# Kernel tuning notes

Hardware: AMD Instinct MI355X
Metric: run time of the kernel (lower is better)

Reference implementation:

```python
import jax, jax.numpy as jnp
import numpy as np

GAMMA = 0.01  # matches init_kwargs gamma
BIG = 1e10    # matches tf.fill(..., 10000000000.0)


def _softmin(vals, gamma):
    # soft-min with softmin weights (my_min in the original): stable log-sum-exp
    z = -vals / gamma
    lse = jax.nn.logsumexp(z)
    return -gamma * lse, jnp.exp(z - lse)


def dtw_grad(theta, gamma):
    """Soft-DTW forward DP + backward E-recursion for one cost matrix theta [m, n].
    Returns E[1:m+1, 1:n+1] (the soft alignment / gradient matrix), shape [m, n]."""
    m, n = theta.shape

    # ---- forward DP: V[i, j] = theta[i-1, j-1] + softmin(V[i,j-1], V[i-1,j-1], V[i-1,j])
    def row_step(prev_row, theta_row):
        # prev_row = V[i-1, 0:n+1]
        def col_step(v_left, inp):
            th, v_diag, v_up = inp
            min_val, w = _softmin(jnp.stack([v_left, v_diag, v_up]), gamma)
            v = th + min_val
            return v, (v, w)
        _, (v_row, q_row) = jax.lax.scan(
            col_step, jnp.float32(BIG), (theta_row, prev_row[:-1], prev_row[1:]))
        new_row = jnp.concatenate([jnp.full((1,), BIG, theta.dtype), v_row])
        return new_row, q_row

    init_row = jnp.full((n + 1,), BIG, theta.dtype).at[0].set(0.0)  # V[0,0]=0
    _, Q_rows = jax.lax.scan(row_step, init_row, theta)  # Q_rows: (m, n, 3)

    # pad Q to (m+2, n+2, 3), Q[m+1, n+1] = [1,1,1]
    Q = (jnp.zeros((m + 2, n + 2, 3), theta.dtype)
         .at[1:m + 1, 1:n + 1].set(Q_rows)
         .at[m + 1, n + 1].set(1.0))

    # ---- backward: E[i,j] = Q[i,j+1,0]E[i,j+1] + Q[i+1,j+1,1]E[i+1,j+1] + Q[i+1,j,2]E[i+1,j]
    def brow_step(e_next, rows):
        # e_next = E[i+1, 0:n+2]; rows = (Q[i], Q[i+1]) each (n+2, 3)
        q_i, q_ip1 = rows
        # j runs n..1 (reverse order along columns)
        xs = (q_i[2:, 0][::-1],        # Q[i, j+1, 0]
              q_ip1[2:, 1][::-1],      # Q[i+1, j+1, 1]
              q_ip1[1:n + 1, 2][::-1], # Q[i+1, j, 2]
              e_next[2:][::-1],        # E[i+1, j+1]
              e_next[1:n + 1][::-1])   # E[i+1, j]

        def bcol_step(e_right, x):
            a, b, c, e1, e2 = x
            e = a * e_right + b * e1 + c * e2
            return e, e

        _, e_rev = jax.lax.scan(bcol_step, jnp.float32(0.0), xs)
        e_inner = e_rev[::-1]  # E[i, 1:n+1]
        e_row = jnp.zeros((n + 2,), theta.dtype).at[1:n + 1].set(e_inner)
        return e_row, e_inner

    e_init = jnp.zeros((n + 2,), theta.dtype).at[n + 1].set(1.0)  # E[m+1, n+1] = 1
    _, E_rev = jax.lax.scan(brow_step, e_init, (Q[m:0:-1], Q[m + 1:1:-1]))
    return E_rev[::-1]  # (m, n)


def setup_inputs() -> dict:
    key = jax.random.key(0)
    # D: batch of pairwise cost matrices, non-negative
    D = jax.random.uniform(key, (64, 256, 256), dtype=jnp.float32)
    return {"D": D}


def reference(D):
    E = jax.vmap(lambda t: dtw_grad(t, GAMMA))(D)  # (B, N, N)
    return jnp.mean(E, axis=0)
```

## Files before the change

kernel.cpp:

```cpp
#include <hip/hip_runtime.h>


#define MM 256
#define NN 256
#define R 2
#define NB 64
#define NBLK 128
#define NVL 128
#define SBIG 1.0e12f
#define K2   144.269504089f

__device__ __forceinline__ float f4get(const float4& v, int k) {
    switch (k) { case 0: return v.x; case 1: return v.y; case 2: return v.z; default: return v.w; }
}
__device__ __forceinline__ int iclamp(int x, int lo, int hi) {
    return x < lo ? lo : (x > hi ? hi : x);
}
__device__ __forceinline__ void lds_barrier() {
    asm volatile("s_waitcnt lgkmcnt(0)\n\ts_barrier" ::: "memory");
}

template<bool REV>
__device__ __forceinline__ void run_dp(const float* __restrict__ th,
                                       float* __restrict__ Vp,
                                       float4 (*xb)[NVL + 1])
{
    const int L = threadIdx.x;

    float vprev[R];
    #pragma unroll
    for (int r = 0; r < R; ++r) vprev[r] = SBIG;
    float4 rec = make_float4(SBIG, SBIG, SBIG, SBIG);
    float prevW = SBIG;
    float4 botV4 = make_float4(SBIG, SBIG, SBIG, SBIG);
    float4 thB[3][R];
    #pragma unroll
    for (int p = 0; p < 3; ++p)
        #pragma unroll
        for (int r = 0; r < R; ++r) thB[p][r] = make_float4(0.f, 0.f, 0.f, 0.f);

    if (threadIdx.x == 0) {
        xb[0][0] = make_float4(SBIG, SBIG, SBIG, SBIG);
        xb[1][0] = make_float4(SBIG, SBIG, SBIG, SBIG);
    }
    __syncthreads();

    auto body = [&](const int LD, const int CU, const int m) {
        const int g = m - L;
        const int gl = iclamp(g + 2, 0, 63);
        #pragma unroll
        for (int r = 0; r < R; ++r) {
            const int vr = 2 * L + r;
            if (REV) {
                const float4 t = *(const float4*)(th + (255 - vr) * NN + (252 - 4 * gl));
                thB[LD][r] = make_float4(t.w, t.z, t.y, t.x);
            } else {
                thB[LD][r] = *(const float4*)(th + vr * NN + 4 * gl);
            }
        }
        if (g >= 0 && g <= 63) {
            const float4 topV = rec;
            const float vd0 = (g == 0) ? ((L == 0) ? 0.0f : SBIG) : prevW;
            float vbuf[R][4];
            #pragma unroll
            for (int cc = 0; cc < 4; ++cc) {
                float vu = f4get(topV, cc);
                float vd = (cc == 0) ? vd0 : f4get(topV, cc - 1);
                #pragma unroll
                for (int r = 0; r < R; ++r) {
                    const float vl = vprev[r];
                    const float mn = fminf(vl, fminf(vd, vu));
                    const float el = exp2f(mn - vl);
                    const float ed = exp2f(mn - vd);
                    const float eu = exp2f(mn - vu);
                    const float ss = el + ed + eu;
                    const float a  = mn - log2f(ss);
                    const float v  = fmaf(f4get(thB[CU][r], cc), K2, a);
                    vbuf[r][cc] = v;
                    vd = vl;
                    vu = v;
                    vprev[r] = v;
                }
            }
            botV4 = make_float4(vbuf[R - 1][0], vbuf[R - 1][1], vbuf[R - 1][2], vbuf[R - 1][3]);
            #pragma unroll
            for (int r = 0; r < R; ++r) {
                const int vr = 2 * L + r;
                if (REV)
                    *(float4*)(Vp + (255 - vr) * NN + (252 - 4 * g)) =
                        make_float4(vbuf[r][3], vbuf[r][2], vbuf[r][1], vbuf[r][0]);
                else
                    *(float4*)(Vp + vr * NN + 4 * g) =
                        make_float4(vbuf[r][0], vbuf[r][1], vbuf[r][2], vbuf[r][3]);
            }
        }
        xb[m & 1][L + 1] = botV4;
        lds_barrier();
        prevW = rec.w;
        rec = xb[m & 1][L];
    };
    for (int k = 0; k < 195; k += 3) {
        body(0, 1, k - 2);
        body(1, 2, k - 1);
        body(2, 0, k);
    }
}

__global__ __launch_bounds__(128) void dtw_fb(
    const float* __restrict__ D,
    float* __restrict__ out,
    float* __restrict__ ws)
{
    __shared__ float4 xb[2][NVL + 1];

    const int blk = blockIdx.x;
    const bool rev = blk >= NB;
    const int b = rev ? blk - NB : blk;
    const float* __restrict__ th = D + (size_t)b * (MM * NN);
    float* __restrict__ Fp = ws + (size_t)b * (MM * NN);
    float* __restrict__ Bp = ws + (size_t)(NB + b) * (MM * NN);
    unsigned* ctr = (unsigned*)(ws + (size_t)2 * NB * (MM * NN));

    if (rev) run_dp<true >(th, Bp, xb);
    else     run_dp<false>(th, Fp, xb);

    __syncthreads();
    __threadfence();
    __syncthreads();
    if (threadIdx.x == 0)
        __hip_atomic_fetch_add(ctr, 1u, __ATOMIC_ACQ_REL, __HIP_MEMORY_SCOPE_AGENT);
    unsigned cnt;
    do {
        cnt = __hip_atomic_load(ctr, __ATOMIC_ACQUIRE, __HIP_MEMORY_SCOPE_AGENT);
        if (cnt < NBLK) __builtin_amdgcn_s_sleep(2);
    } while (cnt < NBLK);
    __builtin_amdgcn_fence(__ATOMIC_ACQUIRE, "agent");

    {
        const int row = 2 * blk + (threadIdx.x >> 6);
        const int col = 4 * (threadIdx.x & 63);
        const size_t off = (size_t)row * NN + col;
        float4 acc = make_float4(0.f, 0.f, 0.f, 0.f);
        for (int p = 0; p < NB; ++p) {
            const float* __restrict__ thp = D + (size_t)p * (MM * NN);
            const float* __restrict__ fp  = ws + (size_t)p * (MM * NN);
            const float* __restrict__ bp  = ws + (size_t)(NB + p) * (MM * NN);
            const float Ft = fp[MM * NN - 1];
            const float4 t4 = *(const float4*)(thp + off);
            const float4 f4 = *(const float4*)(fp + off);
            const float4 b4 = *(const float4*)(bp + off);
            acc.x += exp2f(fmaf(t4.x, K2, (Ft - f4.x) - b4.x));
            acc.y += exp2f(fmaf(t4.y, K2, (Ft - f4.y) - b4.y));
            acc.z += exp2f(fmaf(t4.z, K2, (Ft - f4.z) - b4.z));
            acc.w += exp2f(fmaf(t4.w, K2, (Ft - f4.w) - b4.w));
        }
        const float inv = 1.0f / (float)NB;
        *(float4*)(out + off) =
            make_float4(acc.x * inv, acc.y * inv, acc.z * inv, acc.w * inv);
    }
}

extern "C" void kernel_launch(void* const* d_in, const int* in_sizes, int n_in,
                              void* d_out, int out_size, void* d_ws, size_t ws_size,
                              hipStream_t stream) {
    const float* D = (const float*)d_in[0];
    float* out = (float*)d_out;
    float* ws = (float*)d_ws;

    hipMemsetAsync(ws + (size_t)2 * NB * (MM * NN), 0, sizeof(unsigned), stream);
    dtw_fb<<<dim3(NBLK), dim3(128), 0, stream>>>(D, out, ws);
}
```

Before: 235.9 us.

## Shrink DP to one wavefront with four rows per lane and shuffle handoff

The wavefront DP now runs in a single 64-lane wavefront per block, with each lane owning four rows instead of two. Rows pass between neighbouring lanes through __shfl_up instead of an LDS buffer and block-wide barriers. This cuts the pipeline length from 195 to 129 steps and removes barrier cost on the serial critical path, but each lane now does twice the sequential work per step. The final reduction is reorganised so each thread handles two float4 column chunks to match the smaller block.

```diff
diff --git a/kernel.cpp b/kernel.cpp
--- a/kernel.cpp
+++ b/kernel.cpp
@@ -3,10 +3,9 @@
 
 #define MM 256
 #define NN 256
-#define R 2
+#define R 4
 #define NB 64
 #define NBLK 128
-#define NVL 128
 #define SBIG 1.0e12f
 #define K2   144.269504089f
 
@@ -16,14 +15,10 @@
 __device__ __forceinline__ int iclamp(int x, int lo, int hi) {
     return x < lo ? lo : (x > hi ? hi : x);
 }
-__device__ __forceinline__ void lds_barrier() {
-    asm volatile("s_waitcnt lgkmcnt(0)\n\ts_barrier" ::: "memory");
-}
 
 template<bool REV>
 __device__ __forceinline__ void run_dp(const float* __restrict__ th,
-                                       float* __restrict__ Vp,
-                                       float4 (*xb)[NVL + 1])
+                                       float* __restrict__ Vp)
 {
     const int L = threadIdx.x;
 
@@ -39,18 +34,12 @@
         #pragma unroll
         for (int r = 0; r < R; ++r) thB[p][r] = make_float4(0.f, 0.f, 0.f, 0.f);
 
-    if (threadIdx.x == 0) {
-        xb[0][0] = make_float4(SBIG, SBIG, SBIG, SBIG);
-        xb[1][0] = make_float4(SBIG, SBIG, SBIG, SBIG);
-    }
-    __syncthreads();
-
     auto body = [&](const int LD, const int CU, const int m) {
         const int g = m - L;
         const int gl = iclamp(g + 2, 0, 63);
         #pragma unroll
         for (int r = 0; r < R; ++r) {
-            const int vr = 2 * L + r;
+            const int vr = 4 * L + r;
             if (REV) {
                 const float4 t = *(const float4*)(th + (255 - vr) * NN + (252 - 4 * gl));
                 thB[LD][r] = make_float4(t.w, t.z, t.y, t.x);
@@ -58,7 +47,7 @@
                 thB[LD][r] = *(const float4*)(th + vr * NN + 4 * gl);
             }
         }
-        if (g >= 0 && g <= 63) {
+        if ((unsigned)g <= 63u) {
             const float4 topV = rec;
             const float vd0 = (g == 0) ? ((L == 0) ? 0.0f : SBIG) : prevW;
             float vbuf[R][4];
@@ -85,7 +74,7 @@
             botV4 = make_float4(vbuf[R - 1][0], vbuf[R - 1][1], vbuf[R - 1][2], vbuf[R - 1][3]);
             #pragma unroll
             for (int r = 0; r < R; ++r) {
-                const int vr = 2 * L + r;
+                const int vr = 4 * L + r;
                 if (REV)
                     *(float4*)(Vp + (255 - vr) * NN + (252 - 4 * g)) =
                         make_float4(vbuf[r][3], vbuf[r][2], vbuf[r][1], vbuf[r][0]);
@@ -94,25 +83,27 @@
                         make_float4(vbuf[r][0], vbuf[r][1], vbuf[r][2], vbuf[r][3]);
             }
         }
-        xb[m & 1][L + 1] = botV4;
-        lds_barrier();
+        float4 nr;
+        nr.x = __shfl_up(botV4.x, 1);
+        nr.y = __shfl_up(botV4.y, 1);
+        nr.z = __shfl_up(botV4.z, 1);
+        nr.w = __shfl_up(botV4.w, 1);
         prevW = rec.w;
-        rec = xb[m & 1][L];
+        if (L == 0) nr = make_float4(SBIG, SBIG, SBIG, SBIG);
+        rec = nr;
     };
-    for (int k = 0; k < 195; k += 3) {
+    for (int k = 0; k < 129; k += 3) {
         body(0, 1, k - 2);
         body(1, 2, k - 1);
         body(2, 0, k);
     }
 }
 
-__global__ __launch_bounds__(128) void dtw_fb(
+__global__ __launch_bounds__(64) void dtw_fb(
     const float* __restrict__ D,
     float* __restrict__ out,
     float* __restrict__ ws)
 {
-    __shared__ float4 xb[2][NVL + 1];
-
     const int blk = blockIdx.x;
     const bool rev = blk >= NB;
     const int b = rev ? blk - NB : blk;
@@ -121,12 +112,10 @@
     float* __restrict__ Bp = ws + (size_t)(NB + b) * (MM * NN);
     unsigned* ctr = (unsigned*)(ws + (size_t)2 * NB * (MM * NN));
 
-    if (rev) run_dp<true >(th, Bp, xb);
-    else     run_dp<false>(th, Fp, xb);
+    if (rev) run_dp<true >(th, Bp);
+    else     run_dp<false>(th, Fp);
 
-    __syncthreads();
     __threadfence();
-    __syncthreads();
     if (threadIdx.x == 0)
         __hip_atomic_fetch_add(ctr, 1u, __ATOMIC_ACQ_REL, __HIP_MEMORY_SCOPE_AGENT);
     unsigned cnt;
@@ -137,26 +126,38 @@
     __builtin_amdgcn_fence(__ATOMIC_ACQUIRE, "agent");
 
     {
-        const int row = 2 * blk + (threadIdx.x >> 6);
-        const int col = 4 * (threadIdx.x & 63);
-        const size_t off = (size_t)row * NN + col;
-        float4 acc = make_float4(0.f, 0.f, 0.f, 0.f);
+        const int t = threadIdx.x;
+        const int row = 2 * blk + (t >> 5);
+        const int cb  = 4 * (t & 31);
+        const size_t off0 = (size_t)row * NN + cb;
+        const size_t off1 = off0 + 128;
+        float4 acc0 = make_float4(0.f, 0.f, 0.f, 0.f);
+        float4 acc1 = make_float4(0.f, 0.f, 0.f, 0.f);
         for (int p = 0; p < NB; ++p) {
             const float* __restrict__ thp = D + (size_t)p * (MM * NN);
             const float* __restrict__ fp  = ws + (size_t)p * (MM * NN);
             const float* __restrict__ bp  = ws + (size_t)(NB + p) * (MM * NN);
             const float Ft = fp[MM * NN - 1];
-            const float4 t4 = *(const float4*)(thp + off);
-            const float4 f4 = *(const float4*)(fp + off);
-            const float4 b4 = *(const float4*)(bp + off);
-            acc.x += exp2f(fmaf(t4.x, K2, (Ft - f4.x) - b4.x));
-            acc.y += exp2f(fmaf(t4.y, K2, (Ft - f4.y) - b4.y));
-            acc.z += exp2f(fmaf(t4.z, K2, (Ft - f4.z) - b4.z));
-            acc.w += exp2f(fmaf(t4.w, K2, (Ft - f4.w) - b4.w));
+            const float4 t0 = *(const float4*)(thp + off0);
+            const float4 f0 = *(const float4*)(fp + off0);
+            const float4 b0 = *(const float4*)(bp + off0);
+            acc0.x += exp2f(fmaf(t0.x, K2, (Ft - f0.x) - b0.x));
+            acc0.y += exp2f(fmaf(t0.y, K2, (Ft - f0.y) - b0.y));
+            acc0.z += exp2f(fmaf(t0.z, K2, (Ft - f0.z) - b0.z));
+            acc0.w += exp2f(fmaf(t0.w, K2, (Ft - f0.w) - b0.w));
+            const float4 t1 = *(const float4*)(thp + off1);
+            const float4 f1 = *(const float4*)(fp + off1);
+            const float4 b1 = *(const float4*)(bp + off1);
+            acc1.x += exp2f(fmaf(t1.x, K2, (Ft - f1.x) - b1.x));
+            acc1.y += exp2f(fmaf(t1.y, K2, (Ft - f1.y) - b1.y));
+            acc1.z += exp2f(fmaf(t1.z, K2, (Ft - f1.z) - b1.z));
+            acc1.w += exp2f(fmaf(t1.w, K2, (Ft - f1.w) - b1.w));
         }
         const float inv = 1.0f / (float)NB;
-        *(float4*)(out + off) =
-            make_float4(acc.x * inv, acc.y * inv, acc.z * inv, acc.w * inv);
+        *(float4*)(out + off0) =
+            make_float4(acc0.x * inv, acc0.y * inv, acc0.z * inv, acc0.w * inv);
+        *(float4*)(out + off1) =
+            make_float4(acc1.x * inv, acc1.y * inv, acc1.z * inv, acc1.w * inv);
     }
 }
 
@@ -168,5 +169,5 @@
     float* ws = (float*)d_ws;
 
     hipMemsetAsync(ws + (size_t)2 * NB * (MM * NN), 0, sizeof(unsigned), stream);
-    dtw_fb<<<dim3(NBLK), dim3(128), 0, stream>>>(D, out, ws);
+    dtw_fb<<<dim3(NBLK), dim3(64), 0, stream>>>(D, out, ws);
 }
```

Measured after the change: 268.6 us. 1.14x slower.
